# Performance work log

Measured on AMD Instinct MI355X. Metric: run time of the kernel, lower is better.

## Reference

```python
import jax, jax.numpy as jnp
import numpy as np

EMBED = 512
HEADS = 8
HEAD_DIM = EMBED // HEADS


def setup_inputs() -> dict:
    key = jax.random.key(0)
    ks = jax.random.split(key, 12)
    B, L, D = 2, 4096, EMBED
    s = 1.0 / np.sqrt(D)  # torch Linear default init range scale (approx, uniform)
    def lin(k):
        kw, kb = jax.random.split(k)
        W = jax.random.uniform(kw, (D, D), jnp.float32, -s, s)
        b = jax.random.uniform(kb, (D,), jnp.float32, -s, s)
        return W, b
    Wq, bq = lin(ks[0])
    Wk, bk = lin(ks[1])
    Wv, bv = lin(ks[2])
    Wo, bo = lin(ks[3])
    query = jax.random.normal(ks[4], (B, L, D), jnp.float32)
    key_t = jax.random.normal(ks[5], (B, L, D), jnp.float32)
    value = jax.random.normal(ks[6], (B, L, D), jnp.float32)
    return {"query": query, "key": key_t, "value": value,
            "Wq": Wq, "bq": bq, "Wk": Wk, "bk": bk,
            "Wv": Wv, "bv": bv, "Wo": Wo, "bo": bo}


def reference(query, key, value, Wq, bq, Wk, bk, Wv, bv, Wo, bo):
    B, L, D = query.shape
    H, Hd = HEADS, HEAD_DIM
    scale = Hd ** -0.5
    # torch nn.Linear: y = x @ W.T + b
    q = (query @ Wq.T + bq).reshape(B, L, H, Hd).transpose(0, 2, 1, 3)   # [B,H,L,Hd]
    k = (key   @ Wk.T + bk).reshape(B, -1, H, Hd).transpose(0, 2, 1, 3)
    v = (value @ Wv.T + bv).reshape(B, -1, H, Hd).transpose(0, 2, 1, 3)
    scores = jnp.einsum('bhqd,bhkd->bhqk', q, k) * scale                  # [B,H,L,L]
    causal = jnp.triu(jnp.ones((L, L), dtype=bool), k=1)                  # True above diag
    neg = jnp.finfo(scores.dtype).min
    scores = jnp.where(causal, neg, scores)
    attn = jax.nn.softmax(scores, axis=-1)
    # dropout is identity in eval mode
    out = jnp.einsum('bhqk,bhkd->bhqd', attn, v)                          # [B,H,L,Hd]
    out = out.transpose(0, 2, 1, 3).reshape(B, L, D)
    return out @ Wo.T + bo, attn
```

## Files before the change

kernel.cpp:

```cpp
#include <hip/hip_runtime.h>
#include <hip/hip_bf16.h>


typedef __attribute__((ext_vector_type(8))) __bf16 bf16x8;
typedef __attribute__((ext_vector_type(4))) float f32x4;

constexpr int LL = 4096;
constexpr int DD = 512;
constexpr int HH = 8;
constexpr int HD = 64;
constexpr int BB = 2;
constexpr int BL = BB * LL;
constexpr size_t OUT_ELEMS = (size_t)BB * LL * DD;

static __device__ inline bf16x8 cvt8(const float* p) {
    float4 a = *reinterpret_cast<const float4*>(p);
    float4 b = *reinterpret_cast<const float4*>(p + 4);
    bf16x8 r;
    r[0] = (__bf16)a.x; r[1] = (__bf16)a.y; r[2] = (__bf16)a.z; r[3] = (__bf16)a.w;
    r[4] = (__bf16)b.x; r[5] = (__bf16)b.y; r[6] = (__bf16)b.z; r[7] = (__bf16)b.w;
    return r;
}

static __device__ inline float4 up4(unsigned a, unsigned b) {
    float4 r;
    r.x = __uint_as_float(a << 16);
    r.y = __uint_as_float(a & 0xffff0000u);
    r.z = __uint_as_float(b << 16);
    r.w = __uint_as_float(b & 0xffff0000u);
    return r;
}

__global__ __launch_bounds__(256) void qkv_kernel(
    const float* __restrict__ q_in, const float* __restrict__ k_in,
    const float* __restrict__ v_in,
    const float* __restrict__ Wq, const float* __restrict__ bq,
    const float* __restrict__ Wk, const float* __restrict__ bk,
    const float* __restrict__ Wv, const float* __restrict__ bv,
    __bf16* __restrict__ Qb, __bf16* __restrict__ Kb, __bf16* __restrict__ Vt)
{
    const int z = blockIdx.z;
    const float* x   = (z == 0) ? q_in : (z == 1) ? k_in : v_in;
    const float* W   = (z == 0) ? Wq   : (z == 1) ? Wk   : Wv;
    const float* bia = (z == 0) ? bq   : (z == 1) ? bk   : bv;

    const int wid = threadIdx.x >> 6;
    const int lane = threadIdx.x & 63;
    const int l15 = lane & 15;
    const int lg  = lane >> 4;

    const int r0 = blockIdx.x * 64;
    const int cb = blockIdx.y;
    const int c0 = cb * 64 + wid * 16;

    f32x4 acc[4] = {};
    for (int k0 = 0; k0 < DD; k0 += 32) {
        bf16x8 bfrag = cvt8(&W[(size_t)(c0 + l15) * DD + k0 + lg * 8]);
#pragma unroll
        for (int mt = 0; mt < 4; ++mt) {
            bf16x8 afrag = cvt8(&x[(size_t)(r0 + mt * 16 + l15) * DD + k0 + lg * 8]);
            acc[mt] = __builtin_amdgcn_mfma_f32_16x16x32_bf16(afrag, bfrag, acc[mt], 0, 0, 0);
        }
    }

    __shared__ __bf16 T[64][72];
    const float bval = bia[c0 + l15];
#pragma unroll
    for (int mt = 0; mt < 4; ++mt)
#pragma unroll
        for (int i = 0; i < 4; ++i) {
            const float val = acc[mt][i] + bval;
            const int row = mt * 16 + lg * 4 + i;
            const int col = wid * 16 + l15;
            if (z == 2) T[col][row] = (__bf16)val;
            else        T[row][col] = (__bf16)val;
        }
    __syncthreads();

    const int tr  = threadIdx.x >> 2;
    const int seg = threadIdx.x & 3;
    uint4 v0 = *reinterpret_cast<const uint4*>(&T[tr][seg * 16]);
    uint4 v1 = *reinterpret_cast<const uint4*>(&T[tr][seg * 16 + 8]);
    const int b  = r0 >> 12;
    const int l0 = r0 & (LL - 1);
    if (z == 2) {
        __bf16* dst = Vt + ((size_t)(b * HH + cb) * HD + tr) * LL + l0 + seg * 16;
        *reinterpret_cast<uint4*>(dst)     = v0;
        *reinterpret_cast<uint4*>(dst + 8) = v1;
    } else {
        __bf16* base = (z == 0) ? Qb : Kb;
        __bf16* dst = base + ((size_t)(b * HH + cb) * LL + l0 + tr) * HD + seg * 16;
        *reinterpret_cast<uint4*>(dst)     = v0;
        *reinterpret_cast<uint4*>(dst + 8) = v1;
    }
}

__global__ __launch_bounds__(256) void attn_kernel(
    const __bf16* __restrict__ Qb, const __bf16* __restrict__ Kb,
    const __bf16* __restrict__ Vt, __bf16* __restrict__ Ob,
    float* __restrict__ attn_out)
{
    const int bh = blockIdx.x;
    const int qb = 63 - blockIdx.y;

    const int w    = threadIdx.x >> 6;
    const int lane = threadIdx.x & 63;
    const int l15  = lane & 15;
    const int lg   = lane >> 4;

    const __bf16* Qh = Qb + (size_t)bh * LL * HD;
    const __bf16* Kh = Kb + (size_t)bh * LL * HD;
    const __bf16* Vh = Vt + (size_t)bh * HD * LL;
    float* A_out = attn_out + (size_t)bh * LL * LL;

    __shared__ __bf16 P[4][16][72];

    const int q0 = qb * 64 + w * 16;
    const bf16x8 qf0 = *reinterpret_cast<const bf16x8*>(&Qh[(size_t)(q0 + l15) * HD + lg * 8]);
    const bf16x8 qf1 = *reinterpret_cast<const bf16x8*>(&Qh[(size_t)(q0 + l15) * HD + 32 + lg * 8]);

    const float SC = 0.125f * 1.44269504088896f;

    float rs[4] = {0.f, 0.f, 0.f, 0.f};
    for (int kb = 0; kb <= qb; ++kb) {
        f32x4 s[4] = {};
#pragma unroll
        for (int kt = 0; kt < 4; ++kt) {
            const __bf16* kp = &Kh[(size_t)(kb * 64 + kt * 16 + l15) * HD + lg * 8];
            const bf16x8 k0 = *reinterpret_cast<const bf16x8*>(kp);
            const bf16x8 k1 = *reinterpret_cast<const bf16x8*>(kp + 32);
            s[kt] = __builtin_amdgcn_mfma_f32_16x16x32_bf16(qf0, k0, s[kt], 0, 0, 0);
            s[kt] = __builtin_amdgcn_mfma_f32_16x16x32_bf16(qf1, k1, s[kt], 0, 0, 0);
        }
        if (kb == qb) {
#pragma unroll
            for (int kt = 0; kt < 4; ++kt)
#pragma unroll
                for (int i = 0; i < 4; ++i) {
                    const int kcol = kb * 64 + kt * 16 + l15;
                    const int qrow = q0 + lg * 4 + i;
                    rs[i] += (kcol <= qrow) ? exp2f(s[kt][i] * SC) : 0.f;
                }
        } else {
#pragma unroll
            for (int kt = 0; kt < 4; ++kt)
#pragma unroll
                for (int i = 0; i < 4; ++i)
                    rs[i] += exp2f(s[kt][i] * SC);
        }
    }
#pragma unroll
    for (int off = 1; off < 16; off <<= 1)
#pragma unroll
        for (int i = 0; i < 4; ++i)
            rs[i] += __shfl_xor(rs[i], off, 64);
    float llog[4];
#pragma unroll
    for (int i = 0; i < 4; ++i) llog[i] = -log2f(rs[i]);

    f32x4 oacc[4] = {};
    const int arow = lane >> 2;
    const int aseg = lane & 3;

    for (int kb = 0; kb <= qb; ++kb) {
        f32x4 s[4] = {};
#pragma unroll
        for (int kt = 0; kt < 4; ++kt) {
            const __bf16* kp = &Kh[(size_t)(kb * 64 + kt * 16 + l15) * HD + lg * 8];
            const bf16x8 k0 = *reinterpret_cast<const bf16x8*>(kp);
            const bf16x8 k1 = *reinterpret_cast<const bf16x8*>(kp + 32);
            s[kt] = __builtin_amdgcn_mfma_f32_16x16x32_bf16(qf0, k0, s[kt], 0, 0, 0);
            s[kt] = __builtin_amdgcn_mfma_f32_16x16x32_bf16(qf1, k1, s[kt], 0, 0, 0);
        }
        if (kb == qb) {
#pragma unroll
            for (int kt = 0; kt < 4; ++kt)
#pragma unroll
                for (int i = 0; i < 4; ++i) {
                    const int kcol = kb * 64 + kt * 16 + l15;
                    const int qrow = q0 + lg * 4 + i;
                    float e = exp2f(fmaf(s[kt][i], SC, llog[i]));
                    if (kcol > qrow) e = 0.f;
                    P[w][lg * 4 + i][kt * 16 + l15] = (__bf16)e;
                }
        } else {
#pragma unroll
            for (int kt = 0; kt < 4; ++kt)
#pragma unroll
                for (int i = 0; i < 4; ++i)
                    P[w][lg * 4 + i][kt * 16 + l15] =
                        (__bf16)exp2f(fmaf(s[kt][i], SC, llog[i]));
        }

        {
            uint4 a0 = *reinterpret_cast<const uint4*>(&P[w][arow][aseg * 16]);
            uint4 a1 = *reinterpret_cast<const uint4*>(&P[w][arow][aseg * 16 + 8]);
            float4* dst = reinterpret_cast<float4*>(
                &A_out[(size_t)(q0 + arow) * LL + kb * 64 + aseg * 16]);
            dst[0] = up4(a0.x, a0.y);
            dst[1] = up4(a0.z, a0.w);
            dst[2] = up4(a1.x, a1.y);
            dst[3] = up4(a1.z, a1.w);
        }

        const bf16x8 pa0 = *reinterpret_cast<const bf16x8*>(&P[w][l15][lg * 8]);
        const bf16x8 pa1 = *reinterpret_cast<const bf16x8*>(&P[w][l15][32 + lg * 8]);
#pragma unroll
        for (int ht = 0; ht < 4; ++ht) {
            const __bf16* vp = &Vh[(size_t)(ht * 16 + l15) * LL + kb * 64 + lg * 8];
            const bf16x8 vf0 = *reinterpret_cast<const bf16x8*>(vp);
            const bf16x8 vf1 = *reinterpret_cast<const bf16x8*>(vp + 32);
            oacc[ht] = __builtin_amdgcn_mfma_f32_16x16x32_bf16(pa0, vf0, oacc[ht], 0, 0, 0);
            oacc[ht] = __builtin_amdgcn_mfma_f32_16x16x32_bf16(pa1, vf1, oacc[ht], 0, 0, 0);
        }
    }

    {
#pragma unroll
        for (int ht = 0; ht < 4; ++ht)
#pragma unroll
            for (int i = 0; i < 4; ++i)
                P[w][lg * 4 + i][ht * 16 + l15] = (__bf16)oacc[ht][i];
        uint4 o0 = *reinterpret_cast<const uint4*>(&P[w][arow][aseg * 16]);
        uint4 o1 = *reinterpret_cast<const uint4*>(&P[w][arow][aseg * 16 + 8]);
        const int b = bh >> 3, h = bh & 7;
        __bf16* dst = Ob + ((size_t)(b * LL + q0 + arow)) * DD + h * HD + aseg * 16;
        *reinterpret_cast<uint4*>(dst)     = o0;
        *reinterpret_cast<uint4*>(dst + 8) = o1;
    }

    {
        const int ztr = threadIdx.x >> 2;
        const int zc  = (threadIdx.x & 3) * 16;
        const size_t rowbase = (size_t)(qb * 64 + ztr) * LL;
        const float4 z4 = {0.f, 0.f, 0.f, 0.f};
        for (int c = (qb + 1) * 64 + zc; c < LL; c += 64) {
            float4* d = reinterpret_cast<float4*>(&A_out[rowbase + c]);
            d[0] = z4; d[1] = z4; d[2] = z4; d[3] = z4;
        }
    }
}

__global__ __launch_bounds__(256) void oproj_kernel(
    const __bf16* __restrict__ Ob, const float* __restrict__ Wo,
    const float* __restrict__ bo, float* __restrict__ out)
{
    const int wid = threadIdx.x >> 6;
    const int lane = threadIdx.x & 63;
    const int l15 = lane & 15;
    const int lg  = lane >> 4;

    const int r0 = blockIdx.x * 64;
    const int c0 = blockIdx.y * 64 + wid * 16;

    f32x4 acc[4] = {};
    for (int k0 = 0; k0 < DD; k0 += 32) {
        bf16x8 bfrag = cvt8(&Wo[(size_t)(c0 + l15) * DD + k0 + lg * 8]);
#pragma unroll
        for (int mt = 0; mt < 4; ++mt) {
            bf16x8 afrag = *reinterpret_cast<const bf16x8*>(
                &Ob[(size_t)(r0 + mt * 16 + l15) * DD + k0 + lg * 8]);
            acc[mt] = __builtin_amdgcn_mfma_f32_16x16x32_bf16(afrag, bfrag, acc[mt], 0, 0, 0);
        }
    }
    const float bval = bo[c0 + l15];
#pragma unroll
    for (int mt = 0; mt < 4; ++mt)
#pragma unroll
        for (int i = 0; i < 4; ++i)
            out[(size_t)(r0 + mt * 16 + lg * 4 + i) * DD + c0 + l15] = acc[mt][i] + bval;
}

extern "C" void kernel_launch(void* const* d_in, const int* in_sizes, int n_in,
                              void* d_out, int out_size, void* d_ws, size_t ws_size,
                              hipStream_t stream) {
    const float* query = (const float*)d_in[0];
    const float* key_t = (const float*)d_in[1];
    const float* value = (const float*)d_in[2];
    const float* Wq = (const float*)d_in[3];
    const float* bq = (const float*)d_in[4];
    const float* Wk = (const float*)d_in[5];
    const float* bk = (const float*)d_in[6];
    const float* Wv = (const float*)d_in[7];
    const float* bv = (const float*)d_in[8];
    const float* Wo = (const float*)d_in[9];
    const float* bo = (const float*)d_in[10];

    float* out  = (float*)d_out;
    float* attn = out + OUT_ELEMS;

    char* ws = (char*)d_ws;
    __bf16* Qb = (__bf16*)(ws);
    __bf16* Kb = (__bf16*)(ws + (size_t)8 * 1024 * 1024);
    __bf16* Vt = (__bf16*)(ws + (size_t)16 * 1024 * 1024);
    __bf16* Ob = (__bf16*)(ws + (size_t)24 * 1024 * 1024);

    qkv_kernel<<<dim3(BL / 64, DD / 64, 3), 256, 0, stream>>>(
        query, key_t, value, Wq, bq, Wk, bk, Wv, bv, Qb, Kb, Vt);
    attn_kernel<<<dim3(BB * HH, LL / 64), 256, 0, stream>>>(Qb, Kb, Vt, Ob, attn);
    oproj_kernel<<<dim3(BL / 64, DD / 64), 256, 0, stream>>>(Ob, Wo, bo, out);
}
```

Before: 901.3 us.

## Split attention KV loop across two wave groups, prefetch K, pre-convert inputs

The attention kernel now launches 512 threads, and two groups of four waves each take alternating key blocks. The groups combine their row sums and partial outputs through shared memory. K fragments are double-buffered in registers and V fragments are loaded at the start of each iteration, to hide load latency. A separate kernel converts the fp32 inputs to bf16 once, so the QKV projection no longer reconverts each row for every column block. The score MFMA operands are swapped so the causal mask uses the transposed row layout. This adds a kernel launch, extra workspace traffic and two block-wide syncs.

```diff
diff --git a/kernel.cpp b/kernel.cpp
--- a/kernel.cpp
+++ b/kernel.cpp
@@ -3,6 +3,7 @@
 
 
 typedef __attribute__((ext_vector_type(8))) __bf16 bf16x8;
+typedef __attribute__((ext_vector_type(4))) __bf16 bf16v4;
 typedef __attribute__((ext_vector_type(4))) float f32x4;
 
 constexpr int LL = 4096;
@@ -31,18 +32,29 @@
     return r;
 }
 
+__global__ __launch_bounds__(256) void cvt_kernel(
+    const float* __restrict__ q, const float* __restrict__ k,
+    const float* __restrict__ v, __bf16* __restrict__ o)
+{
+    constexpr size_t N = (size_t)BL * DD;
+    size_t i = ((size_t)blockIdx.x * 256 + threadIdx.x) * 8;
+    const float* src = q; size_t j = i;
+    if (i >= 2 * N)      { src = v; j = i - 2 * N; }
+    else if (i >= N)     { src = k; j = i - N; }
+    *reinterpret_cast<bf16x8*>(&o[i]) = cvt8(&src[j]);
+}
+
 __global__ __launch_bounds__(256) void qkv_kernel(
-    const float* __restrict__ q_in, const float* __restrict__ k_in,
-    const float* __restrict__ v_in,
+    const __bf16* __restrict__ Xb,
     const float* __restrict__ Wq, const float* __restrict__ bq,
     const float* __restrict__ Wk, const float* __restrict__ bk,
     const float* __restrict__ Wv, const float* __restrict__ bv,
     __bf16* __restrict__ Qb, __bf16* __restrict__ Kb, __bf16* __restrict__ Vt)
 {
     const int z = blockIdx.z;
-    const float* x   = (z == 0) ? q_in : (z == 1) ? k_in : v_in;
-    const float* W   = (z == 0) ? Wq   : (z == 1) ? Wk   : Wv;
-    const float* bia = (z == 0) ? bq   : (z == 1) ? bk   : bv;
+    const __bf16* x  = Xb + (size_t)z * BL * DD;
+    const float* W   = (z == 0) ? Wq : (z == 1) ? Wk : Wv;
+    const float* bia = (z == 0) ? bq : (z == 1) ? bk : bv;
 
     const int wid = threadIdx.x >> 6;
     const int lane = threadIdx.x & 63;
@@ -58,7 +70,8 @@
         bf16x8 bfrag = cvt8(&W[(size_t)(c0 + l15) * DD + k0 + lg * 8]);
 #pragma unroll
         for (int mt = 0; mt < 4; ++mt) {
-            bf16x8 afrag = cvt8(&x[(size_t)(r0 + mt * 16 + l15) * DD + k0 + lg * 8]);
+            bf16x8 afrag = *reinterpret_cast<const bf16x8*>(
+                &x[(size_t)(r0 + mt * 16 + l15) * DD + k0 + lg * 8]);
             acc[mt] = __builtin_amdgcn_mfma_f32_16x16x32_bf16(afrag, bfrag, acc[mt], 0, 0, 0);
         }
     }
@@ -95,7 +108,7 @@
     }
 }
 
-__global__ __launch_bounds__(256) void attn_kernel(
+__global__ __launch_bounds__(512, 3) void attn_kernel(
     const __bf16* __restrict__ Qb, const __bf16* __restrict__ Kb,
     const __bf16* __restrict__ Vt, __bf16* __restrict__ Ob,
     float* __restrict__ attn_out)
@@ -103,7 +116,9 @@
     const int bh = blockIdx.x;
     const int qb = 63 - blockIdx.y;
 
-    const int w    = threadIdx.x >> 6;
+    const int wv   = threadIdx.x >> 6;
+    const int wr   = wv & 3;
+    const int par  = wv >> 2;
     const int lane = threadIdx.x & 63;
     const int l15  = lane & 15;
     const int lg   = lane >> 4;
@@ -113,88 +128,95 @@
     const __bf16* Vh = Vt + (size_t)bh * HD * LL;
     float* A_out = attn_out + (size_t)bh * LL * LL;
 
-    __shared__ __bf16 P[4][16][72];
-
-    const int q0 = qb * 64 + w * 16;
+    __shared__ __bf16 P[8][16][72];
+    __shared__ float rsum[2][64];
+
+    const int q0 = qb * 64 + wr * 16;
+    const int qrow = q0 + l15;
     const bf16x8 qf0 = *reinterpret_cast<const bf16x8*>(&Qh[(size_t)(q0 + l15) * HD + lg * 8]);
     const bf16x8 qf1 = *reinterpret_cast<const bf16x8*>(&Qh[(size_t)(q0 + l15) * HD + 32 + lg * 8]);
 
     const float SC = 0.125f * 1.44269504088896f;
 
-    float rs[4] = {0.f, 0.f, 0.f, 0.f};
-    for (int kb = 0; kb <= qb; ++kb) {
+    auto loadK = [&](bf16x8 (&kf)[8], int kb) {
+        const __bf16* kp = &Kh[((size_t)kb * 64 + l15) * HD + lg * 8];
+#pragma unroll
+        for (int kt = 0; kt < 4; ++kt) {
+            kf[kt * 2]     = *reinterpret_cast<const bf16x8*>(kp + (size_t)kt * 16 * HD);
+            kf[kt * 2 + 1] = *reinterpret_cast<const bf16x8*>(kp + (size_t)kt * 16 * HD + 32);
+        }
+    };
+
+    float rs = 0.f;
+    auto body1 = [&](bf16x8 (&kf)[8], int kb) {
         f32x4 s[4] = {};
 #pragma unroll
         for (int kt = 0; kt < 4; ++kt) {
-            const __bf16* kp = &Kh[(size_t)(kb * 64 + kt * 16 + l15) * HD + lg * 8];
-            const bf16x8 k0 = *reinterpret_cast<const bf16x8*>(kp);
-            const bf16x8 k1 = *reinterpret_cast<const bf16x8*>(kp + 32);
-            s[kt] = __builtin_amdgcn_mfma_f32_16x16x32_bf16(qf0, k0, s[kt], 0, 0, 0);
-            s[kt] = __builtin_amdgcn_mfma_f32_16x16x32_bf16(qf1, k1, s[kt], 0, 0, 0);
-        }
-        if (kb == qb) {
-#pragma unroll
-            for (int kt = 0; kt < 4; ++kt)
-#pragma unroll
-                for (int i = 0; i < 4; ++i) {
-                    const int kcol = kb * 64 + kt * 16 + l15;
-                    const int qrow = q0 + lg * 4 + i;
-                    rs[i] += (kcol <= qrow) ? exp2f(s[kt][i] * SC) : 0.f;
-                }
-        } else {
-#pragma unroll
-            for (int kt = 0; kt < 4; ++kt)
-#pragma unroll
-                for (int i = 0; i < 4; ++i)
-                    rs[i] += exp2f(s[kt][i] * SC);
-        }
-    }
-#pragma unroll
-    for (int off = 1; off < 16; off <<= 1)
-#pragma unroll
-        for (int i = 0; i < 4; ++i)
-            rs[i] += __shfl_xor(rs[i], off, 64);
-    float llog[4];
-#pragma unroll
-    for (int i = 0; i < 4; ++i) llog[i] = -log2f(rs[i]);
+            s[kt] = __builtin_amdgcn_mfma_f32_16x16x32_bf16(kf[kt * 2],     qf0, s[kt], 0, 0, 0);
+            s[kt] = __builtin_amdgcn_mfma_f32_16x16x32_bf16(kf[kt * 2 + 1], qf1, s[kt], 0, 0, 0);
+        }
+        const bool diag = (kb == qb);
+#pragma unroll
+        for (int kt = 0; kt < 4; ++kt)
+#pragma unroll
+            for (int i = 0; i < 4; ++i) {
+                float e = exp2f(s[kt][i] * SC);
+                if (diag && (kb * 64 + kt * 16 + lg * 4 + i) > qrow) e = 0.f;
+                rs += e;
+            }
+    };
+    {
+        bf16x8 kA[8], kB[8];
+        int kb = par;
+        bool useA = true;
+        if (kb <= qb) loadK(kA, kb);
+        for (; kb <= qb; kb += 2) {
+            if (useA) { if (kb + 2 <= qb) loadK(kB, kb + 2); body1(kA, kb); }
+            else      { if (kb + 2 <= qb) loadK(kA, kb + 2); body1(kB, kb); }
+            useA = !useA;
+        }
+    }
+    rs += __shfl_xor(rs, 16, 64);
+    rs += __shfl_xor(rs, 32, 64);
+    if (lane < 16) rsum[par][wr * 16 + l15] = rs;
+    __syncthreads();
+    const float llog = -log2f(rsum[0][wr * 16 + l15] + rsum[1][wr * 16 + l15]);
 
     f32x4 oacc[4] = {};
     const int arow = lane >> 2;
     const int aseg = lane & 3;
 
-    for (int kb = 0; kb <= qb; ++kb) {
+    auto body2 = [&](bf16x8 (&kf)[8], int kb) {
+        bf16x8 vf[8];
+        {
+            const __bf16* vp = &Vh[(size_t)l15 * LL + (size_t)kb * 64 + lg * 8];
+#pragma unroll
+            for (int ht = 0; ht < 4; ++ht) {
+                vf[ht * 2]     = *reinterpret_cast<const bf16x8*>(vp + (size_t)ht * 16 * LL);
+                vf[ht * 2 + 1] = *reinterpret_cast<const bf16x8*>(vp + (size_t)ht * 16 * LL + 32);
+            }
+        }
         f32x4 s[4] = {};
 #pragma unroll
         for (int kt = 0; kt < 4; ++kt) {
-            const __bf16* kp = &Kh[(size_t)(kb * 64 + kt * 16 + l15) * HD + lg * 8];
-            const bf16x8 k0 = *reinterpret_cast<const bf16x8*>(kp);
-            const bf16x8 k1 = *reinterpret_cast<const bf16x8*>(kp + 32);
-            s[kt] = __builtin_amdgcn_mfma_f32_16x16x32_bf16(qf0, k0, s[kt], 0, 0, 0);
-            s[kt] = __builtin_amdgcn_mfma_f32_16x16x32_bf16(qf1, k1, s[kt], 0, 0, 0);
-        }
-        if (kb == qb) {
-#pragma unroll
-            for (int kt = 0; kt < 4; ++kt)
-#pragma unroll
-                for (int i = 0; i < 4; ++i) {
-                    const int kcol = kb * 64 + kt * 16 + l15;
-                    const int qrow = q0 + lg * 4 + i;
-                    float e = exp2f(fmaf(s[kt][i], SC, llog[i]));
-                    if (kcol > qrow) e = 0.f;
-                    P[w][lg * 4 + i][kt * 16 + l15] = (__bf16)e;
-                }
-        } else {
-#pragma unroll
-            for (int kt = 0; kt < 4; ++kt)
-#pragma unroll
-                for (int i = 0; i < 4; ++i)
-                    P[w][lg * 4 + i][kt * 16 + l15] =
-                        (__bf16)exp2f(fmaf(s[kt][i], SC, llog[i]));
-        }
-
+            s[kt] = __builtin_amdgcn_mfma_f32_16x16x32_bf16(kf[kt * 2],     qf0, s[kt], 0, 0, 0);
+            s[kt] = __builtin_amdgcn_mfma_f32_16x16x32_bf16(kf[kt * 2 + 1], qf1, s[kt], 0, 0, 0);
+        }
+        const bool diag = (kb == qb);
+#pragma unroll
+        for (int kt = 0; kt < 4; ++kt) {
+            bf16v4 pk;
+#pragma unroll
+            for (int i = 0; i < 4; ++i) {
+                float e = exp2f(fmaf(s[kt][i], SC, llog));
+                if (diag && (kb * 64 + kt * 16 + lg * 4 + i) > qrow) e = 0.f;
+                pk[i] = (__bf16)e;
+            }
+            *reinterpret_cast<bf16v4*>(&P[wv][l15][kt * 16 + lg * 4]) = pk;
+        }
         {
-            uint4 a0 = *reinterpret_cast<const uint4*>(&P[w][arow][aseg * 16]);
-            uint4 a1 = *reinterpret_cast<const uint4*>(&P[w][arow][aseg * 16 + 8]);
+            uint4 a0 = *reinterpret_cast<const uint4*>(&P[wv][arow][aseg * 16]);
+            uint4 a1 = *reinterpret_cast<const uint4*>(&P[wv][arow][aseg * 16 + 8]);
             float4* dst = reinterpret_cast<float4*>(
                 &A_out[(size_t)(q0 + arow) * LL + kb * 64 + aseg * 16]);
             dst[0] = up4(a0.x, a0.y);
@@ -202,27 +224,47 @@
             dst[2] = up4(a1.x, a1.y);
             dst[3] = up4(a1.z, a1.w);
         }
-
-        const bf16x8 pa0 = *reinterpret_cast<const bf16x8*>(&P[w][l15][lg * 8]);
-        const bf16x8 pa1 = *reinterpret_cast<const bf16x8*>(&P[w][l15][32 + lg * 8]);
+        const bf16x8 pa0 = *reinterpret_cast<const bf16x8*>(&P[wv][l15][lg * 8]);
+        const bf16x8 pa1 = *reinterpret_cast<const bf16x8*>(&P[wv][l15][32 + lg * 8]);
 #pragma unroll
         for (int ht = 0; ht < 4; ++ht) {
-            const __bf16* vp = &Vh[(size_t)(ht * 16 + l15) * LL + kb * 64 + lg * 8];
-            const bf16x8 vf0 = *reinterpret_cast<const bf16x8*>(vp);
-            const bf16x8 vf1 = *reinterpret_cast<const bf16x8*>(vp + 32);
-            oacc[ht] = __builtin_amdgcn_mfma_f32_16x16x32_bf16(pa0, vf0, oacc[ht], 0, 0, 0);
-            oacc[ht] = __builtin_amdgcn_mfma_f32_16x16x32_bf16(pa1, vf1, oacc[ht], 0, 0, 0);
-        }
-    }
-
+            oacc[ht] = __builtin_amdgcn_mfma_f32_16x16x32_bf16(pa0, vf[ht * 2],     oacc[ht], 0, 0, 0);
+            oacc[ht] = __builtin_amdgcn_mfma_f32_16x16x32_bf16(pa1, vf[ht * 2 + 1], oacc[ht], 0, 0, 0);
+        }
+    };
     {
+        bf16x8 kA[8], kB[8];
+        int kb = par;
+        bool useA = true;
+        if (kb <= qb) loadK(kA, kb);
+        for (; kb <= qb; kb += 2) {
+            if (useA) { if (kb + 2 <= qb) loadK(kB, kb + 2); body2(kA, kb); }
+            else      { if (kb + 2 <= qb) loadK(kA, kb + 2); body2(kB, kb); }
+            useA = !useA;
+        }
+    }
+
+    if (par == 1) {
 #pragma unroll
         for (int ht = 0; ht < 4; ++ht)
 #pragma unroll
             for (int i = 0; i < 4; ++i)
-                P[w][lg * 4 + i][ht * 16 + l15] = (__bf16)oacc[ht][i];
-        uint4 o0 = *reinterpret_cast<const uint4*>(&P[w][arow][aseg * 16]);
-        uint4 o1 = *reinterpret_cast<const uint4*>(&P[w][arow][aseg * 16 + 8]);
+                P[wv][lg * 4 + i][ht * 16 + l15] = (__bf16)oacc[ht][i];
+    }
+    __syncthreads();
+    if (par == 0) {
+#pragma unroll
+        for (int ht = 0; ht < 4; ++ht)
+#pragma unroll
+            for (int i = 0; i < 4; ++i)
+                oacc[ht][i] += (float)P[wv + 4][lg * 4 + i][ht * 16 + l15];
+#pragma unroll
+        for (int ht = 0; ht < 4; ++ht)
+#pragma unroll
+            for (int i = 0; i < 4; ++i)
+                P[wv][lg * 4 + i][ht * 16 + l15] = (__bf16)oacc[ht][i];
+        uint4 o0 = *reinterpret_cast<const uint4*>(&P[wv][arow][aseg * 16]);
+        uint4 o1 = *reinterpret_cast<const uint4*>(&P[wv][arow][aseg * 16 + 8]);
         const int b = bh >> 3, h = bh & 7;
         __bf16* dst = Ob + ((size_t)(b * LL + q0 + arow)) * DD + h * HD + aseg * 16;
         *reinterpret_cast<uint4*>(dst)     = o0;
@@ -230,11 +272,11 @@
     }
 
     {
-        const int ztr = threadIdx.x >> 2;
-        const int zc  = (threadIdx.x & 3) * 16;
+        const int ztr  = threadIdx.x >> 3;
+        const int zseg = threadIdx.x & 7;
         const size_t rowbase = (size_t)(qb * 64 + ztr) * LL;
         const float4 z4 = {0.f, 0.f, 0.f, 0.f};
-        for (int c = (qb + 1) * 64 + zc; c < LL; c += 64) {
+        for (int c = (qb + 1) * 64 + zseg * 16; c < LL; c += 128) {
             float4* d = reinterpret_cast<float4*>(&A_out[rowbase + c]);
             d[0] = z4; d[1] = z4; d[2] = z4; d[3] = z4;
         }
@@ -294,9 +336,11 @@
     __bf16* Kb = (__bf16*)(ws + (size_t)8 * 1024 * 1024);
     __bf16* Vt = (__bf16*)(ws + (size_t)16 * 1024 * 1024);
     __bf16* Ob = (__bf16*)(ws + (size_t)24 * 1024 * 1024);
-
+    __bf16* Xb = (__bf16*)(ws + (size_t)32 * 1024 * 1024);
+
+    cvt_kernel<<<dim3(3 * BL * DD / 8 / 256), 256, 0, stream>>>(query, key_t, value, Xb);
     qkv_kernel<<<dim3(BL / 64, DD / 64, 3), 256, 0, stream>>>(
-        query, key_t, value, Wq, bq, Wk, bk, Wv, bv, Qb, Kb, Vt);
-    attn_kernel<<<dim3(BB * HH, LL / 64), 256, 0, stream>>>(Qb, Kb, Vt, Ob, attn);
+        Xb, Wq, bq, Wk, bk, Wv, bv, Qb, Kb, Vt);
+    attn_kernel<<<dim3(BB * HH, LL / 64), 512, 0, stream>>>(Qb, Kb, Vt, Ob, attn);
     oproj_kernel<<<dim3(BL / 64, DD / 64), 256, 0, stream>>>(Ob, Wo, bo, out);
 }
```

After: 854.0 us. 1.06x faster.
